# Kernel optimization log

Measured on AMD Instinct MI355X. Metric: run time of the kernel, lower is better.

## Reference

```python
import jax, jax.numpy as jnp
import numpy as np

EPS = 1e-06


def setup_inputs() -> dict:
    key = jax.random.key(0)
    kq, kk, kv = jax.random.split(key, 3)
    shape = (4, 16, 4096, 64)  # [batch, heads, seq, head_dim]
    q = jax.random.normal(kq, shape, dtype=jnp.float32)
    k = jax.random.normal(kk, shape, dtype=jnp.float32)
    v = jax.random.normal(kv, shape, dtype=jnp.float32)
    return {"q": q, "k": k, "v": v}


def reference(q, k, v):
    # elu(x)+1 feature map (positive kernel)
    q_prime = jax.nn.elu(q) + 1.0  # [b,h,s,d]
    k_prime = jax.nn.elu(k) + 1.0  # [b,h,s,d]
    # KV aggregate: [b,h,d,d] -- avoids the [s,s] score matrix
    kv_agg = jnp.einsum('bhsd,bhse->bhde', k_prime, v)
    num = jnp.einsum('bhsd,bhde->bhse', q_prime, kv_agg)  # [b,h,s,d]
    k_sum = k_prime.sum(axis=-2)                           # [b,h,d]
    denom = jnp.einsum('bhsd,bhd->bhs', q_prime, k_sum)[..., None] + EPS
    return num / denom
```

## Files before the change

kernel.cpp:

```cpp
#include <hip/hip_runtime.h>


#define EPS_LA 1e-6f

constexpr int BH = 64;
constexpr int SEQ = 4096;
constexpr int DIM = 64;
constexpr int KVELEM = DIM * DIM + DIM;
constexpr int NPB = 32;
constexpr int SCH = SEQ / NPB;

typedef short bf16x8 __attribute__((ext_vector_type(8)));
typedef float f32x4 __attribute__((ext_vector_type(4)));

__device__ __forceinline__ float elu1(float x) {
    return x > 0.f ? x + 1.f : __expf(x);
}
__device__ __forceinline__ f32x4 elu4v(f32x4 v) {
    v[0] = elu1(v[0]); v[1] = elu1(v[1]); v[2] = elu1(v[2]); v[3] = elu1(v[3]);
    return v;
}
__device__ __forceinline__ f32x4 ntld(const float* p) {
    return __builtin_nontemporal_load((const f32x4*)p);
}

__device__ __forceinline__ unsigned int f2bf(float x) {
    unsigned int u = __float_as_uint(x);
    return (u + 0x7fffu + ((u >> 16) & 1u)) >> 16;
}
__device__ __forceinline__ unsigned int pack2bf(float lo, float hi) {
    return f2bf(lo) | (f2bf(hi) << 16);
}

__device__ __forceinline__ int swz(int d, int s2) {
    return d * 64 + (s2 ^ ((((d >> 1) ^ (d >> 2)) & 7) << 2));
}

template<bool ATOMIC>
__global__ __launch_bounds__(256, 2) void kv_mfma_kernel(
    const float* __restrict__ K, const float* __restrict__ V,
    float* __restrict__ dst) {
    const int bh = blockIdx.y;
    const int blk = blockIdx.x;
    const int t = threadIdx.x;
    const int w = t >> 6, l = t & 63;

    __shared__ unsigned int KT[64 * 64];
    __shared__ unsigned int VT[64 * 64];
    __shared__ float csumS[4][64];

    const float* Kb = K + ((size_t)bh * SEQ + (size_t)blk * SCH) * DIM;
    const float* Vb = V + ((size_t)bh * SEQ + (size_t)blk * SCH) * DIM;

    const int c0 = (t & 15) * 4;
    const int pg = t >> 4;
    const int lg = l >> 4;
    const int lr = l & 15;

    f32x4 kf[8], vf[8];
    #pragma unroll
    for (int i = 0; i < 4; ++i) {
        const int p = pg + 16 * i;
        kf[2 * i]     = ntld(Kb + (size_t)(2 * p) * DIM + c0);
        kf[2 * i + 1] = ntld(Kb + (size_t)(2 * p + 1) * DIM + c0);
    }
    #pragma unroll
    for (int i = 0; i < 4; ++i) {
        const int p = pg + 16 * i;
        vf[2 * i]     = ntld(Vb + (size_t)(2 * p) * DIM + c0);
        vf[2 * i + 1] = ntld(Vb + (size_t)(2 * p + 1) * DIM + c0);
    }

    float cs0 = 0.f, cs1 = 0.f, cs2 = 0.f, cs3 = 0.f;
    #pragma unroll
    for (int i = 0; i < 4; ++i) {
        const int p = pg + 16 * i;
        const f32x4 ka = elu4v(kf[2 * i]);
        const f32x4 kb = elu4v(kf[2 * i + 1]);
        cs0 += ka[0] + kb[0]; cs1 += ka[1] + kb[1];
        cs2 += ka[2] + kb[2]; cs3 += ka[3] + kb[3];
        KT[swz(c0 + 0, p)] = pack2bf(ka[0], kb[0]);
        KT[swz(c0 + 1, p)] = pack2bf(ka[1], kb[1]);
        KT[swz(c0 + 2, p)] = pack2bf(ka[2], kb[2]);
        KT[swz(c0 + 3, p)] = pack2bf(ka[3], kb[3]);
        const f32x4 va = vf[2 * i], vb = vf[2 * i + 1];
        VT[swz(c0 + 0, p)] = pack2bf(va[0], vb[0]);
        VT[swz(c0 + 1, p)] = pack2bf(va[1], vb[1]);
        VT[swz(c0 + 2, p)] = pack2bf(va[2], vb[2]);
        VT[swz(c0 + 3, p)] = pack2bf(va[3], vb[3]);
    }

    cs0 += __shfl_xor(cs0, 16); cs0 += __shfl_xor(cs0, 32);
    cs1 += __shfl_xor(cs1, 16); cs1 += __shfl_xor(cs1, 32);
    cs2 += __shfl_xor(cs2, 16); cs2 += __shfl_xor(cs2, 32);
    cs3 += __shfl_xor(cs3, 16); cs3 += __shfl_xor(cs3, 32);
    if (l < 16) *(f32x4*)&csumS[w][l * 4] = f32x4{cs0, cs1, cs2, cs3};

    __syncthreads();

    f32x4 acc[4];
    #pragma unroll
    for (int m = 0; m < 4; ++m)
        #pragma unroll
        for (int r = 0; r < 4; ++r) acc[m][r] = 0.f;

    #pragma unroll
    for (int ks = 0; ks < 4; ++ks) {
        const int s2b = ks * 16 + lg * 4;
        const bf16x8 bfrag =
            *reinterpret_cast<const bf16x8*>(&VT[swz(16 * w + lr, s2b)]);
        #pragma unroll
        for (int m = 0; m < 4; ++m) {
            const bf16x8 afrag =
                *reinterpret_cast<const bf16x8*>(&KT[swz(16 * m + lr, s2b)]);
            acc[m] = __builtin_amdgcn_mfma_f32_16x16x32_bf16(afrag, bfrag, acc[m],
                                                             0, 0, 0);
        }
    }

    float* wout = ATOMIC ? dst + (size_t)bh * KVELEM
                         : dst + ((size_t)blk * BH + bh) * KVELEM;

    if (t < 64) {
        const float s = csumS[0][t] + csumS[1][t] + csumS[2][t] + csumS[3][t];
        if (ATOMIC) atomicAdd(&wout[DIM * DIM + t], s);
        else        wout[DIM * DIM + t] = s;
    }

    #pragma unroll
    for (int m = 0; m < 4; ++m) {
        #pragma unroll
        for (int r = 0; r < 4; ++r) {
            const int d = 16 * m + 4 * lg + r;
            const int e = 16 * w + lr;
            if (ATOMIC) atomicAdd(&wout[(size_t)d * DIM + e], acc[m][r]);
            else        wout[(size_t)d * DIM + e] = acc[m][r];
        }
    }
}

__global__ __launch_bounds__(256) void reduce_partials_kernel(
    const float* __restrict__ partial, float* __restrict__ fin) {
    const int bh = blockIdx.y;
    const int j = blockIdx.x * 256 + threadIdx.x;
    if (j >= KVELEM) return;
    float s = 0.f;
    #pragma unroll
    for (int c = 0; c < NPB; ++c)
        s += partial[((size_t)c * BH + bh) * KVELEM + j];
    fin[(size_t)bh * KVELEM + j] = s;
}

__global__ __launch_bounds__(256) void out_kernel(
    const float* __restrict__ Q, const float* __restrict__ ws,
    float* __restrict__ out) {
    const int bh = blockIdx.y;
    const int rb = blockIdx.x;
    const int t = threadIdx.x;
    const int wv = t >> 6, l = t & 63;
    const int lr = l & 15, lg = l >> 4;

    __shared__ unsigned int qA[4 * 32 * 32];
    __shared__ unsigned int kvT[64 * 32];
    __shared__ float denomS[128];

    const float* kvp = ws + (size_t)bh * KVELEM;
    const float* Qb = Q + ((size_t)bh * SEQ + (size_t)rb * 128) * DIM;
    float* Ob = out + ((size_t)bh * SEQ + (size_t)rb * 128) * DIM;

    #pragma unroll
    for (int i = 0; i < 2; ++i) {
        const int p = (t >> 4) + 16 * i;
        const int e0 = (t & 15) * 4;
        const f32x4 a = *(const f32x4*)(kvp + (size_t)(2 * p) * DIM + e0);
        const f32x4 b = *(const f32x4*)(kvp + (size_t)(2 * p + 1) * DIM + e0);
        #pragma unroll
        for (int j = 0; j < 4; ++j) {
            const int e = e0 + j;
            kvT[e * 32 + (p ^ ((e & 7) << 2))] = pack2bf(a[j], b[j]);
        }
    }

    const int c0 = lr * 4;
    const f32x4 ks4 = *(const f32x4*)(kvp + DIM * DIM + c0);
    float pd[8];
    #pragma unroll
    for (int it = 0; it < 8; ++it) {
        const int row = it * 4 + lg;
        const f32x4 qv = elu4v(ntld(Qb + (size_t)(wv * 32 + row) * DIM + c0));
        pd[it] = qv[0] * ks4[0] + qv[1] * ks4[1] + qv[2] * ks4[2] + qv[3] * ks4[3];
        uint2 val;
        val.x = pack2bf(qv[0], qv[1]);
        val.y = pack2bf(qv[2], qv[3]);
        *(uint2*)&qA[wv * 1024 + row * 32 + ((2 * lr) ^ ((row & 7) << 2))] = val;
    }
    #pragma unroll
    for (int it = 0; it < 8; ++it) {
        float v = pd[it];
        v += __shfl_xor(v, 1); v += __shfl_xor(v, 2);
        v += __shfl_xor(v, 4); v += __shfl_xor(v, 8);
        if (lr == 0) denomS[wv * 32 + it * 4 + lg] = v + EPS_LA;
    }
    __syncthreads();

    f32x4 acc[2][4];
    #pragma unroll
    for (int mt = 0; mt < 2; ++mt)
        #pragma unroll
        for (int nt = 0; nt < 4; ++nt)
            #pragma unroll
            for (int r = 0; r < 4; ++r) acc[mt][nt][r] = 0.f;

    #pragma unroll
    for (int ks = 0; ks < 2; ++ks) {
        const int kd = 4 * lg + 16 * ks;
        const int am = (lr & 7) << 2;
        const bf16x8 a0 = *(const bf16x8*)&qA[wv * 1024 + lr * 32 + (kd ^ am)];
        const bf16x8 a1 = *(const bf16x8*)&qA[wv * 1024 + (16 + lr) * 32 + (kd ^ am)];
        #pragma unroll
        for (int nt = 0; nt < 4; ++nt) {
            const bf16x8 b =
                *(const bf16x8*)&kvT[(16 * nt + lr) * 32 + (kd ^ am)];
            acc[0][nt] = __builtin_amdgcn_mfma_f32_16x16x32_bf16(a0, b, acc[0][nt],
                                                                 0, 0, 0);
            acc[1][nt] = __builtin_amdgcn_mfma_f32_16x16x32_bf16(a1, b, acc[1][nt],
                                                                 0, 0, 0);
        }
    }

    #pragma unroll
    for (int mt = 0; mt < 2; ++mt) {
        #pragma unroll
        for (int r = 0; r < 4; ++r) {
            const int row = 16 * mt + 4 * lg + r;
            const float inv = 1.f / denomS[wv * 32 + row];
            float* orow = Ob + (size_t)(wv * 32 + row) * DIM;
            #pragma unroll
            for (int nt = 0; nt < 4; ++nt) {
                __builtin_nontemporal_store(acc[mt][nt][r] * inv,
                                            orow + 16 * nt + lr);
            }
        }
    }
}

extern "C" void kernel_launch(void* const* d_in, const int* in_sizes, int n_in,
                              void* d_out, int out_size, void* d_ws, size_t ws_size,
                              hipStream_t stream) {
    const float* q = (const float*)d_in[0];
    const float* k = (const float*)d_in[1];
    const float* v = (const float*)d_in[2];
    float* out = (float*)d_out;
    float* ws = (float*)d_ws;

    const size_t partial_elems = (size_t)NPB * BH * KVELEM;
    const size_t need = (partial_elems + (size_t)BH * KVELEM) * sizeof(float);

    dim3 blk(256);
    const float* fin_ptr;
    if (ws_size >= need) {
        float* partial = ws;
        float* fin = ws + partial_elems;
        hipLaunchKernelGGL((kv_mfma_kernel<false>), dim3(NPB, BH), blk, 0, stream,
                           k, v, partial);
        hipLaunchKernelGGL(reduce_partials_kernel, dim3((KVELEM + 255) / 256, BH),
                           blk, 0, stream, partial, fin);
        fin_ptr = fin;
    } else {
        float* fin = ws;
        hipMemsetAsync(fin, 0, (size_t)BH * KVELEM * sizeof(float), stream);
        hipLaunchKernelGGL((kv_mfma_kernel<true>), dim3(NPB, BH), blk, 0, stream,
                           k, v, fin);
        fin_ptr = fin;
    }
    hipLaunchKernelGGL(out_kernel, dim3(SEQ / 128, BH), blk, 0, stream,
                       q, fin_ptr, out);
}
```

Measured before the change: 69.74 us.

## Vectorize partial reduction, stage output through LDS, raise KV occupancy

The partial-sum reduction now reads and writes float4 vectors instead of scalars. The output kernel stages each 16-row tile in swizzled shared memory so the global stores become coalesced 16-byte nontemporal stores rather than scattered scalar stores. The KV kernel's launch bound is raised to request 4 blocks per SM, which may force register spilling. The staging adds extra barriers and shared-memory traffic.

```diff
diff --git a/kernel.cpp b/kernel.cpp
--- a/kernel.cpp
+++ b/kernel.cpp
@@ -37,7 +37,7 @@
 }
 
 template<bool ATOMIC>
-__global__ __launch_bounds__(256, 2) void kv_mfma_kernel(
+__global__ __launch_bounds__(256, 4) void kv_mfma_kernel(
     const float* __restrict__ K, const float* __restrict__ V,
     float* __restrict__ dst) {
     const int bh = blockIdx.y;
@@ -142,13 +142,13 @@
 __global__ __launch_bounds__(256) void reduce_partials_kernel(
     const float* __restrict__ partial, float* __restrict__ fin) {
     const int bh = blockIdx.y;
-    const int j = blockIdx.x * 256 + threadIdx.x;
-    if (j >= KVELEM) return;
-    float s = 0.f;
+    const int j4 = blockIdx.x * 256 + threadIdx.x;
+    if (j4 >= KVELEM / 4) return;
+    f32x4 s = {0.f, 0.f, 0.f, 0.f};
     #pragma unroll
     for (int c = 0; c < NPB; ++c)
-        s += partial[((size_t)c * BH + bh) * KVELEM + j];
-    fin[(size_t)bh * KVELEM + j] = s;
+        s += *(const f32x4*)&partial[((size_t)c * BH + bh) * KVELEM + j4 * 4];
+    *(f32x4*)&fin[(size_t)bh * KVELEM + j4 * 4] = s;
 }
 
 __global__ __launch_bounds__(256) void out_kernel(
@@ -228,18 +228,29 @@
         }
     }
 
+    float* oS = (float*)qA;
     #pragma unroll
     for (int mt = 0; mt < 2; ++mt) {
+        __syncthreads();
         #pragma unroll
         for (int r = 0; r < 4; ++r) {
-            const int row = 16 * mt + 4 * lg + r;
-            const float inv = 1.f / denomS[wv * 32 + row];
-            float* orow = Ob + (size_t)(wv * 32 + row) * DIM;
+            const int row = 4 * lg + r;
+            const float inv = 1.f / denomS[wv * 32 + mt * 16 + row];
             #pragma unroll
             for (int nt = 0; nt < 4; ++nt) {
-                __builtin_nontemporal_store(acc[mt][nt][r] * inv,
-                                            orow + 16 * nt + lr);
+                const int colp = (16 * nt + lr) ^ (lg << 4);
+                oS[wv * 1024 + row * 64 + colp] = acc[mt][nt][r] * inv;
             }
+        }
+        __syncthreads();
+        #pragma unroll
+        for (int j = 0; j < 4; ++j) {
+            const int row = 4 * j + lg;
+            const int cb = lr * 4;
+            const int colp = cb ^ ((row >> 2) << 4);
+            const f32x4 o = *(const f32x4*)&oS[wv * 1024 + row * 64 + colp];
+            float* orow = Ob + (size_t)(wv * 32 + mt * 16 + row) * DIM + cb;
+            __builtin_nontemporal_store(o, (f32x4*)orow);
         }
     }
 }
@@ -263,7 +274,7 @@
         float* fin = ws + partial_elems;
         hipLaunchKernelGGL((kv_mfma_kernel<false>), dim3(NPB, BH), blk, 0, stream,
                            k, v, partial);
-        hipLaunchKernelGGL(reduce_partials_kernel, dim3((KVELEM + 255) / 256, BH),
+        hipLaunchKernelGGL(reduce_partials_kernel, dim3((KVELEM / 4 + 255) / 256, BH),
                            blk, 0, stream, partial, fin);
         fin_ptr = fin;
     } else {
```

Measured after the change: 67.76 us. -2.8%, faster.
